# Kernel optimization log

Hardware: AMD Instinct MI355X
Metric: run time of the kernel (lower is better)

## Reference

```python
import jax, jax.numpy as jnp
import numpy as np

N = 25000      # nodes
E = 400000     # edges (avg degree 16)
D = 128        # input feature dim
H = 4          # heads in layer 1
O1 = 128       # per-head out dim layer 1
O2 = 64        # out dim layer 2 (1 head)
NG = 512       # number of graphs in batch
NEG_SLOPE = 0.2


def _gat_layer(x, src, dst, W, a_src, a_dst, bias, heads, out_dim):
    """PyG-style GATConv: gather, per-edge logits, segment softmax over dst, scatter-add."""
    n = x.shape[0]
    h = (x @ W).reshape(n, heads, out_dim)              # [N,H,O]
    al_s = jnp.sum(h * a_src, axis=-1)                  # [N,H]
    al_d = jnp.sum(h * a_dst, axis=-1)                  # [N,H]
    e = jax.nn.leaky_relu(al_s[src] + al_d[dst], NEG_SLOPE)   # [E,H]
    e_max = jax.ops.segment_max(e, dst, num_segments=n)        # [N,H]
    e_exp = jnp.exp(e - e_max[dst])
    denom = jax.ops.segment_sum(e_exp, dst, num_segments=n)    # [N,H]
    alpha = e_exp / denom[dst]                                  # [E,H]
    msg = alpha[:, :, None] * h[src]                             # [E,H,O]  (dominant traffic)
    out = jax.ops.segment_sum(msg, dst, num_segments=n)         # [N,H,O]
    return out.reshape(n, heads * out_dim) + bias


def setup_inputs() -> dict:
    key = jax.random.key(0)
    ks = jax.random.split(key, 16)
    x = jax.random.normal(ks[0], (N, D), dtype=jnp.float32)
    edge_index = jax.random.randint(ks[1], (2, E), 0, N, dtype=jnp.int64)
    batch = jnp.sort(jax.random.randint(ks[2], (N,), 0, NG, dtype=jnp.int64))
    def glorot(k, shape, fan_in):
        return jax.random.normal(k, shape, dtype=jnp.float32) * (1.0 / np.sqrt(fan_in))
    W1 = glorot(ks[3], (D, H * O1), D)
    a_src1 = glorot(ks[4], (H, O1), O1)
    a_dst1 = glorot(ks[5], (H, O1), O1)
    b1 = jnp.zeros((H * O1,), dtype=jnp.float32)
    W2 = glorot(ks[6], (H * O1, O2), H * O1)
    a_src2 = glorot(ks[7], (1, O2), O2)
    a_dst2 = glorot(ks[8], (1, O2), O2)
    b2 = jnp.zeros((O2,), dtype=jnp.float32)
    fc_w1 = glorot(ks[9], (O2, 32), O2)
    fc_b1 = jnp.zeros((32,), dtype=jnp.float32)
    fc_w2 = glorot(ks[10], (32, 1), 32)
    fc_b2 = jnp.zeros((1,), dtype=jnp.float32)
    return {"x": x, "edge_index": edge_index, "batch": batch,
            "W1": W1, "a_src1": a_src1, "a_dst1": a_dst1, "b1": b1,
            "W2": W2, "a_src2": a_src2, "a_dst2": a_dst2, "b2": b2,
            "fc_w1": fc_w1, "fc_b1": fc_b1, "fc_w2": fc_w2, "fc_b2": fc_b2}


def reference(x, edge_index, batch, W1, a_src1, a_dst1, b1, W2, a_src2, a_dst2, b2,
              fc_w1, fc_b1, fc_w2, fc_b2):
    n = x.shape[0]
    loop = jnp.arange(n, dtype=edge_index.dtype)
    src = jnp.concatenate([edge_index[0], loop])   # add_self_loops=True (PyG default)
    dst = jnp.concatenate([edge_index[1], loop])
    h1 = jax.nn.elu(_gat_layer(x, src, dst, W1, a_src1, a_dst1, b1, H, O1))   # [N, 512]
    h2 = jax.nn.elu(_gat_layer(h1, src, dst, W2, a_src2, a_dst2, b2, 1, O2))  # [N, 64]
    # global mean pool over graphs
    sums = jax.ops.segment_sum(h2, batch, num_segments=NG)                     # [NG, 64]
    cnt = jax.ops.segment_sum(jnp.ones((n,), dtype=h2.dtype), batch, num_segments=NG)
    pooled = sums / jnp.maximum(cnt, 1.0)[:, None]
    hid = jax.nn.relu(pooled @ fc_w1 + fc_b1)
    out = jax.nn.sigmoid(hid @ fc_w2 + fc_b2)
    return out.squeeze(-1)                                                     # [NG]
```

## Files before the change

kernel.cpp:

```cpp
#include <hip/hip_runtime.h>
#include <hip/hip_bf16.h>


typedef unsigned short u16;
typedef unsigned int u32;
typedef __attribute__((ext_vector_type(8))) short bf16x8;
typedef __attribute__((ext_vector_type(4))) float f32x4;

#define LRELU(v) ((v) > 0.0f ? (v) : 0.2f * (v))
#define ELU(v)   ((v) > 0.0f ? (v) : expm1f(v))

__device__ __forceinline__ u16 f2bf(float f) {
    union { float f; u32 u; } c; c.f = f;
    u32 u = c.u;
    u32 r = (u + 0x7fffu + ((u >> 16) & 1u)) >> 16;
    return (u16)r;
}
__device__ __forceinline__ float bf2f(u16 h) {
    return __uint_as_float(((u32)h) << 16);
}

__global__ __launch_bounds__(256) void prep_w(const float* __restrict__ W1,
                                              const float* __restrict__ W2,
                                              const float* __restrict__ a_s,
                                              const float* __restrict__ a_d,
                                              u16* __restrict__ W1f,
                                              u16* __restrict__ W2f,
                                              float* __restrict__ Wa,
                                              int* __restrict__ deg, int nDeg) {
    int b = blockIdx.x;
    if (b < 384) {
        int idx = b * 256 + threadIdx.x;
        if (idx < 65536) {
            int fid = idx >> 9, l = (idx >> 3) & 63, j = idx & 7;
            int head = fid >> 5, cb = (fid >> 2) & 7, s = fid & 3;
            int col = head * 128 + cb * 16 + (l & 15);
            int k = s * 32 + 16 * (j >> 2) + 4 * (l >> 4) + (j & 3);
            W1f[idx] = f2bf(W1[(size_t)k * 512 + col]);
        } else {
            int i2 = idx - 65536;
            int fid = i2 >> 9, l = (i2 >> 3) & 63, j = i2 & 7;
            int c2 = fid >> 4, s = fid & 15;
            int col = c2 * 16 + (l & 15);
            int k = s * 32 + 16 * (j >> 2) + 4 * (l >> 4) + (j & 3);
            W2f[i2] = f2bf(W2[(size_t)k * 64 + col]);
        }
    } else if (b < 388) {
        int idx = (b - 384) * 256 + threadIdx.x;
        int k = idx >> 3, j = idx & 7, h = j & 3;
        const float* a = (j < 4) ? (a_s + h * 128) : (a_d + h * 128);
        const float* wrow = W1 + (size_t)k * 512 + h * 128;
        float s = 0.f;
#pragma unroll 8
        for (int o = 0; o < 128; ++o) s += wrow[o] * a[o];
        Wa[k * 8 + j] = s;
    } else {
        int i = (b - 388) * 1024 + threadIdx.x * 4;
        if (i < nDeg) *(int4*)(deg + i) = make_int4(0, 0, 0, 0);
    }
}

__global__ __launch_bounds__(256) void prep_x(const float* __restrict__ x,
                                              const float* __restrict__ Wa,
                                              const int* __restrict__ dstA,
                                              u16* __restrict__ xbf,
                                              float* __restrict__ alS,
                                              float* __restrict__ alD,
                                              int* __restrict__ deg,
                                              int Nn, int E, int NBx) {
    int b = blockIdx.x;
    if (b >= NBx) {
        int e = (b - NBx) * 256 + threadIdx.x;
        if (e < E + Nn) {
            int d = (e < E) ? dstA[e] : (e - E);
            atomicAdd(&deg[d], 1);
        }
        return;
    }
    int lane = threadIdx.x & 63;
    int wave = threadIdx.x >> 6;
    float4 ls = *(const float4*)(Wa + lane * 8);
    float4 ld = *(const float4*)(Wa + lane * 8 + 4);
    float4 hs = *(const float4*)(Wa + (lane + 64) * 8);
    float4 hd = *(const float4*)(Wa + (lane + 64) * 8 + 4);
    int n = b * 4 + wave;
    if (n >= Nn) return;
    float x0 = x[(size_t)n * 128 + lane];
    float x1 = x[(size_t)n * 128 + lane + 64];
    xbf[(size_t)n * 128 + lane]      = f2bf(x0);
    xbf[(size_t)n * 128 + lane + 64] = f2bf(x1);
    float r0 = x0 * ls.x + x1 * hs.x;
    float r1 = x0 * ls.y + x1 * hs.y;
    float r2 = x0 * ls.z + x1 * hs.z;
    float r3 = x0 * ls.w + x1 * hs.w;
    float r4 = x0 * ld.x + x1 * hd.x;
    float r5 = x0 * ld.y + x1 * hd.y;
    float r6 = x0 * ld.z + x1 * hd.z;
    float r7 = x0 * ld.w + x1 * hd.w;
#pragma unroll
    for (int off = 32; off; off >>= 1) {
        r0 += __shfl_down(r0, off); r1 += __shfl_down(r1, off);
        r2 += __shfl_down(r2, off); r3 += __shfl_down(r3, off);
        r4 += __shfl_down(r4, off); r5 += __shfl_down(r5, off);
        r6 += __shfl_down(r6, off); r7 += __shfl_down(r7, off);
    }
    if (lane == 0) {
        *(float4*)(alS + (size_t)n * 4) = make_float4(r0, r1, r2, r3);
        *(float4*)(alD + (size_t)n * 4) = make_float4(r4, r5, r6, r7);
    }
}

__global__ __launch_bounds__(256) void scanA_kernel(const int* __restrict__ deg,
                                                    int* __restrict__ offs,
                                                    int* __restrict__ bsum, int n) {
    __shared__ int sh[256];
    int b = blockIdx.x, t = threadIdx.x;
    int base = b * 2048 + t * 8;
    int v[8]; int s = 0;
#pragma unroll
    for (int j = 0; j < 8; ++j) { int i = base + j; v[j] = (i < n) ? deg[i] : 0; s += v[j]; }
    sh[t] = s;
    __syncthreads();
    for (int off = 1; off < 256; off <<= 1) {
        int u = (t >= off) ? sh[t - off] : 0;
        __syncthreads();
        sh[t] += u;
        __syncthreads();
    }
    int run = sh[t] - s;
    if (t == 255) bsum[b] = sh[255];
#pragma unroll
    for (int j = 0; j < 8; ++j) {
        run += v[j];
        int i = base + j;
        if (i < n) offs[i + 1] = run;
    }
}

__global__ __launch_bounds__(256) void scanC_kernel(int* __restrict__ offs,
                                                    const int* __restrict__ bsum, int n) {
    int i = blockIdx.x * 256 + threadIdx.x;
    if (i == 0) offs[0] = 0;
    if (i >= n) return;
    int b = i >> 11;
    int add = 0;
    for (int j = 0; j < b; ++j) add += bsum[j];
    if (b > 0) offs[i + 1] += add;
}

__global__ __launch_bounds__(256) void scatter_kernel(const int* __restrict__ src,
                                                      const int* __restrict__ dst,
                                                      int E, int Nn,
                                                      const int* __restrict__ offs,
                                                      int* __restrict__ fill,
                                                      const float* __restrict__ alS,
                                                      const float* __restrict__ alD,
                                                      int* __restrict__ sCSR,
                                                      float* __restrict__ wE1) {
    int e = blockIdx.x * 256 + threadIdx.x;
    if (e >= E + Nn) return;
    int s = (e < E) ? src[e] : (e - E);
    int d = (e < E) ? dst[e] : (e - E);
    int pos = offs[d] + atomicAdd(&fill[d], 1);
    sCSR[pos] = s;
    float4 as = *(const float4*)(alS + (size_t)s * 4);
    float4 ad = *(const float4*)(alD + (size_t)d * 4);
    float4 w;
    float t;
    t = as.x + ad.x; w.x = expf(LRELU(t));
    t = as.y + ad.y; w.y = expf(LRELU(t));
    t = as.z + ad.z; w.z = expf(LRELU(t));
    t = as.w + ad.w; w.w = expf(LRELU(t));
    *(float4*)(wE1 + (size_t)pos * 4) = w;
}

__global__ __launch_bounds__(256) void aggx_kernel(const u16* __restrict__ xbf,
                                                   const int* __restrict__ sCSR,
                                                   const int* __restrict__ offs,
                                                   const float* __restrict__ wE,
                                                   u16* __restrict__ xaggF, int Nn) {
    int n = blockIdx.x * 4 + (threadIdx.x >> 6);
    int l = threadIdx.x & 63;
    if (n >= Nn) return;
    int half = l >> 5;
    int fl = (l & 31) * 4;
    float a0[4] = {0.f, 0.f, 0.f, 0.f};
    float a1[4] = {0.f, 0.f, 0.f, 0.f};
    float a2[4] = {0.f, 0.f, 0.f, 0.f};
    float a3[4] = {0.f, 0.f, 0.f, 0.f};
    float ws0 = 0.f, ws1 = 0.f, ws2 = 0.f, ws3 = 0.f;
    int s0 = offs[n], s1 = offs[n + 1];
    int i = s0 + half;
    for (; i + 6 < s1; i += 8) {
        int sn[4]; float4 w[4]; ushort4 u[4];
#pragma unroll
        for (int j = 0; j < 4; ++j) {
            int idx = i + 2 * j;
            sn[j] = sCSR[idx];
            w[j] = *(const float4*)(wE + (size_t)idx * 4);
        }
#pragma unroll
        for (int j = 0; j < 4; ++j)
            u[j] = *(const ushort4*)(xbf + (size_t)sn[j] * 128 + fl);
#pragma unroll
        for (int j = 0; j < 4; ++j) {
            float xv[4] = {bf2f(u[j].x), bf2f(u[j].y), bf2f(u[j].z), bf2f(u[j].w)};
#pragma unroll
            for (int q = 0; q < 4; ++q) {
                a0[q] += w[j].x * xv[q];
                a1[q] += w[j].y * xv[q];
                a2[q] += w[j].z * xv[q];
                a3[q] += w[j].w * xv[q];
            }
            ws0 += w[j].x; ws1 += w[j].y; ws2 += w[j].z; ws3 += w[j].w;
        }
    }
    for (; i < s1; i += 2) {
        int sn = sCSR[i];
        float4 w = *(const float4*)(wE + (size_t)i * 4);
        ushort4 u = *(const ushort4*)(xbf + (size_t)sn * 128 + fl);
        float xv[4] = {bf2f(u.x), bf2f(u.y), bf2f(u.z), bf2f(u.w)};
#pragma unroll
        for (int q = 0; q < 4; ++q) {
            a0[q] += w.x * xv[q];
            a1[q] += w.y * xv[q];
            a2[q] += w.z * xv[q];
            a3[q] += w.w * xv[q];
        }
        ws0 += w.x; ws1 += w.y; ws2 += w.z; ws3 += w.w;
    }
#pragma unroll
    for (int q = 0; q < 4; ++q) {
        a0[q] += __shfl_xor(a0[q], 32);
        a1[q] += __shfl_xor(a1[q], 32);
        a2[q] += __shfl_xor(a2[q], 32);
        a3[q] += __shfl_xor(a3[q], 32);
    }
    ws0 += __shfl_xor(ws0, 32); ws1 += __shfl_xor(ws1, 32);
    ws2 += __shfl_xor(ws2, 32); ws3 += __shfl_xor(ws3, 32);
    if (half == 0) {
        float i0 = 1.f / ws0, i1 = 1.f / ws1, i2 = 1.f / ws2, i3 = 1.f / ws3;
        int group = n >> 4, lrow = n & 15;
        int sl = fl >> 5;
        int kg = (fl >> 2) & 3;
        int j0 = ((fl >> 4) & 1) * 4;
        size_t base = ((size_t)group * 16 + sl) * 512 + (size_t)(kg * 16 + lrow) * 8 + j0;
        ushort4 o;
        o.x = f2bf(a0[0] * i0); o.y = f2bf(a0[1] * i0);
        o.z = f2bf(a0[2] * i0); o.w = f2bf(a0[3] * i0);
        *(ushort4*)(xaggF + base + 0 * 2048) = o;
        o.x = f2bf(a1[0] * i1); o.y = f2bf(a1[1] * i1);
        o.z = f2bf(a1[2] * i1); o.w = f2bf(a1[3] * i1);
        *(ushort4*)(xaggF + base + 1 * 2048) = o;
        o.x = f2bf(a2[0] * i2); o.y = f2bf(a2[1] * i2);
        o.z = f2bf(a2[2] * i2); o.w = f2bf(a2[3] * i2);
        *(ushort4*)(xaggF + base + 2 * 2048) = o;
        o.x = f2bf(a3[0] * i3); o.y = f2bf(a3[1] * i3);
        o.z = f2bf(a3[2] * i3); o.w = f2bf(a3[3] * i3);
        *(ushort4*)(xaggF + base + 3 * 2048) = o;
    }
}

__global__ __launch_bounds__(64) void gemm1_mfma(const u16* __restrict__ xaggF,
                                                 const u16* __restrict__ W1f,
                                                 const float* __restrict__ b1,
                                                 u16* __restrict__ out1F) {
    int l = threadIdx.x;
    int head = blockIdx.y;
    int g0 = blockIdx.x * 2;
    int kg = l >> 4;

    bf16x8 xf[2][4];
#pragma unroll
    for (int g = 0; g < 2; ++g) {
        const u16* p = xaggF + ((size_t)(g0 + g) * 16 + head * 4) * 512 + l * 8;
#pragma unroll
        for (int s = 0; s < 4; ++s) xf[g][s] = *(const bf16x8*)(p + s * 512);
    }

    const u16* wbase = W1f + (size_t)head * 32 * 512 + l * 8;

#pragma unroll
    for (int cbp = 0; cbp < 4; ++cbp) {
        bf16x8 op0, op1;
#pragma unroll
        for (int par = 0; par < 2; ++par) {
            int cb = cbp * 2 + par;
            bf16x8 wf[4];
#pragma unroll
            for (int s = 0; s < 4; ++s)
                wf[s] = *(const bf16x8*)(wbase + (size_t)(cb * 4 + s) * 512);
            float4 bias = *(const float4*)(b1 + head * 128 + cb * 16 + kg * 4);
#pragma unroll
            for (int g = 0; g < 2; ++g) {
                f32x4 acc = {0.f, 0.f, 0.f, 0.f};
#pragma unroll
                for (int s = 0; s < 4; ++s)
                    acc = __builtin_amdgcn_mfma_f32_16x16x32_bf16(wf[s], xf[g][s],
                                                                  acc, 0, 0, 0);
                float v0 = ELU(acc[0] + bias.x);
                float v1 = ELU(acc[1] + bias.y);
                float v2 = ELU(acc[2] + bias.z);
                float v3 = ELU(acc[3] + bias.w);
                bf16x8& op = g ? op1 : op0;
                if (par == 0) {
                    op[0] = (short)f2bf(v0); op[1] = (short)f2bf(v1);
                    op[2] = (short)f2bf(v2); op[3] = (short)f2bf(v3);
                } else {
                    op[4] = (short)f2bf(v0); op[5] = (short)f2bf(v1);
                    op[6] = (short)f2bf(v2); op[7] = (short)f2bf(v3);
                }
            }
        }
#pragma unroll
        for (int g = 0; g < 2; ++g) {
            u16* op = out1F + ((size_t)(g0 + g) * 16 + head * 4 + cbp) * 512 + l * 8;
            *(bf16x8*)op = g ? op1 : op0;
        }
    }
}

__global__ __launch_bounds__(64) void gemm2_mfma(const u16* __restrict__ out1F,
                                                 const u16* __restrict__ W2f,
                                                 const float* __restrict__ a_s2,
                                                 const float* __restrict__ a_d2,
                                                 u16* __restrict__ h2bf,
                                                 float* __restrict__ alS,
                                                 float* __restrict__ alD, int M) {
    int l = threadIdx.x;
    int g = blockIdx.x;
    int lrow = l & 15, kg = l >> 4;
    int node = g * 16 + lrow;

    const u16* xp = out1F + (size_t)g * 16 * 512 + l * 8;
    bf16x8 xf[16];
#pragma unroll
    for (int s = 0; s < 16; ++s) xf[s] = *(const bf16x8*)(xp + s * 512);

    const u16* wp = W2f + l * 8;
    float ps = 0.f, pd = 0.f;
#pragma unroll
    for (int c2 = 0; c2 < 4; ++c2) {
        int c0 = c2 * 16;
        f32x4 acc = {0.f, 0.f, 0.f, 0.f};
#pragma unroll
        for (int s = 0; s < 16; ++s) {
            bf16x8 wf = *(const bf16x8*)(wp + (size_t)(c2 * 16 + s) * 512);
            acc = __builtin_amdgcn_mfma_f32_16x16x32_bf16(wf, xf[s], acc, 0, 0, 0);
        }
        float4 as = *(const float4*)(a_s2 + c0 + kg * 4);
        float4 ad = *(const float4*)(a_d2 + c0 + kg * 4);
        ps += acc[0] * as.x + acc[1] * as.y + acc[2] * as.z + acc[3] * as.w;
        pd += acc[0] * ad.x + acc[1] * ad.y + acc[2] * ad.z + acc[3] * ad.w;
        if (node < M) {
            ushort4 o;
            o.x = f2bf(acc[0]); o.y = f2bf(acc[1]);
            o.z = f2bf(acc[2]); o.w = f2bf(acc[3]);
            *(ushort4*)(h2bf + (size_t)node * 64 + c0 + kg * 4) = o;
        }
    }
    ps += __shfl_xor(ps, 16); ps += __shfl_xor(ps, 32);
    pd += __shfl_xor(pd, 16); pd += __shfl_xor(pd, 32);
    if (kg == 0 && node < M) { alS[node] = ps; alD[node] = pd; }
}

__global__ __launch_bounds__(256) void agg2_kernel(const u16* __restrict__ h2bf,
                                                   const int* __restrict__ sCSR,
                                                   const int* __restrict__ offs,
                                                   const float* __restrict__ alS2,
                                                   const float* __restrict__ alD2,
                                                   const float* __restrict__ b2,
                                                   float* __restrict__ out2, int Nn) {
    int n = blockIdx.x * 4 + (threadIdx.x >> 6);
    int l = threadIdx.x & 63;
    if (n >= Nn) return;
    int half = l >> 5;
    int fl = (l & 31) * 2;
    float ad = alD2[n];
    float ax = 0.f, ay = 0.f, ws = 0.f;
    int s0 = offs[n], s1 = offs[n + 1];
    int i = s0 + half;
    for (; i + 6 < s1; i += 8) {
        int sn[4]; float als[4]; u32 u[4];
#pragma unroll
        for (int j = 0; j < 4; ++j) sn[j] = sCSR[i + 2 * j];
#pragma unroll
        for (int j = 0; j < 4; ++j) {
            als[j] = alS2[sn[j]];
            u[j] = *(const u32*)(h2bf + (size_t)sn[j] * 64 + fl);
        }
#pragma unroll
        for (int j = 0; j < 4; ++j) {
            float t = als[j] + ad;
            float w = expf(LRELU(t));
            ax += w * __uint_as_float(u[j] << 16);
            ay += w * __uint_as_float(u[j] & 0xffff0000u);
            ws += w;
        }
    }
    for (; i < s1; i += 2) {
        int sn = sCSR[i];
        float t = alS2[sn] + ad;
        float w = expf(LRELU(t));
        u32 u = *(const u32*)(h2bf + (size_t)sn * 64 + fl);
        ax += w * __uint_as_float(u << 16);
        ay += w * __uint_as_float(u & 0xffff0000u);
        ws += w;
    }
    ax += __shfl_xor(ax, 32);
    ay += __shfl_xor(ay, 32);
    ws += __shfl_xor(ws, 32);
    if (half == 0) {
        float inv = 1.f / ws;
        float2 o;
        float v0 = ax * inv + b2[fl];
        float v1 = ay * inv + b2[fl + 1];
        o.x = ELU(v0);
        o.y = ELU(v1);
        *(float2*)(out2 + (size_t)n * 64 + fl) = o;
    }
}

__device__ __forceinline__ int lower_bound_i(const int* arr, int n, int key) {
    int lo = 0, hi = n;
    while (lo < hi) {
        int mid = (lo + hi) >> 1;
        if (arr[mid] < key) lo = mid + 1; else hi = mid;
    }
    return lo;
}

__global__ __launch_bounds__(64) void poolfc_kernel(const float* __restrict__ h2,
                                                    const int* __restrict__ batch,
                                                    int Nn,
                                                    const float* __restrict__ w1,
                                                    const float* __restrict__ bb1,
                                                    const float* __restrict__ w2,
                                                    const float* __restrict__ bb2,
                                                    float* __restrict__ out) {
    int g = blockIdx.x;
    __shared__ int sh[2];
    __shared__ float p[64];
    __shared__ float hid[32];
    int t = threadIdx.x;
    if (t == 0) sh[0] = lower_bound_i(batch, Nn, g);
    if (t == 1) sh[1] = lower_bound_i(batch, Nn, g + 1);
    __syncthreads();
    int s0 = sh[0], s1 = sh[1];
    float sum = 0.f;
    for (int i = s0; i < s1; ++i) sum += h2[(size_t)i * 64 + t];
    float cnt = (float)((s1 - s0) > 1 ? (s1 - s0) : 1);
    p[t] = sum / cnt;
    __syncthreads();
    if (t < 32) {
        float a = bb1[t];
#pragma unroll
        for (int k = 0; k < 64; ++k) a += p[k] * w1[k * 32 + t];
        hid[t] = a > 0.f ? a : 0.f;
    }
    __syncthreads();
    if (t == 0) {
        float a = bb2[0];
#pragma unroll
        for (int j = 0; j < 32; ++j) a += hid[j] * w2[j];
        out[g] = 1.0f / (1.0f + expf(-a));
    }
}

extern "C" void kernel_launch(void* const* d_in, const int* in_sizes, int n_in,
                              void* d_out, int out_size, void* d_ws, size_t ws_size,
                              hipStream_t stream) {
    const float* x      = (const float*)d_in[0];
    const int*   ei     = (const int*)d_in[1];
    const int*   batch  = (const int*)d_in[2];
    const float* W1     = (const float*)d_in[3];
    const float* a_src1 = (const float*)d_in[4];
    const float* a_dst1 = (const float*)d_in[5];
    const float* b1     = (const float*)d_in[6];
    const float* W2     = (const float*)d_in[7];
    const float* a_src2 = (const float*)d_in[8];
    const float* a_dst2 = (const float*)d_in[9];
    const float* b2     = (const float*)d_in[10];
    const float* fcw1   = (const float*)d_in[11];
    const float* fcb1   = (const float*)d_in[12];
    const float* fcw2   = (const float*)d_in[13];
    const float* fcb2   = (const float*)d_in[14];
    float* out = (float*)d_out;

    const int Nn = in_sizes[0] / 128;
    const int E  = in_sizes[1] / 2;
    const int Et = E + Nn;
    const int NG = out_size;
    const int* srcA = ei;
    const int* dstA = ei + E;

    const int ngroups = (Nn + 15) / 16;
    const int ngp = (ngroups + 1) & ~1;

    char* base = (char*)d_ws;
    size_t off = 0;
    auto alloc = [&](size_t bytes) -> void* {
        void* p = base + off;
        off += (bytes + 255) & ~(size_t)255;
        return p;
    };
    u16*   xbf    = (u16*)alloc((size_t)Nn * 128 * 2);
    u16*   xaggF  = (u16*)alloc((size_t)ngp * 16 * 512 * 2);
    u16*   out1F  = (u16*)alloc((size_t)ngp * 16 * 512 * 2);
    u16*   h2bf   = (u16*)alloc((size_t)Nn * 64 * 2);
    float* out2   = (float*)alloc((size_t)Nn * 64 * 4);
    u16*   W1f    = (u16*)alloc(65536 * 2);
    u16*   W2f    = (u16*)alloc(32768 * 2);
    float* Wa     = (float*)alloc(128 * 8 * 4);
    float* alS1   = (float*)alloc((size_t)Nn * 4 * 4);
    float* alD1   = (float*)alloc((size_t)Nn * 4 * 4);
    float* alS2   = (float*)alloc((size_t)Nn * 4);
    float* alD2   = (float*)alloc((size_t)Nn * 4);
    float* wE1    = (float*)alloc((size_t)Et * 4 * 4);
    int*   deg    = (int*)alloc((size_t)2 * Nn * 4);
    int*   fill   = deg + Nn;
    int*   offs   = (int*)alloc((size_t)(Nn + 1) * 4);
    int*   bsum   = (int*)alloc(64 * 4);
    int*   sCSR   = (int*)alloc((size_t)Et * 4);
    (void)ws_size; (void)n_in;

    const int EB = (Et + 255) / 256;
    const int NB = (Nn + 2047) / 2048;
    const int NBx = (Nn + 3) / 4;
    const int ZB = (2 * Nn + 1023) / 1024;

    prep_w<<<388 + ZB, 256, 0, stream>>>(W1, W2, a_src1, a_dst1, W1f, W2f, Wa,
                                         deg, 2 * Nn);
    prep_x<<<NBx + EB, 256, 0, stream>>>(x, Wa, dstA, xbf, alS1, alD1, deg,
                                         Nn, E, NBx);
    scanA_kernel<<<NB, 256, 0, stream>>>(deg, offs, bsum, Nn);
    scanC_kernel<<<(Nn + 255) / 256, 256, 0, stream>>>(offs, bsum, Nn);
    scatter_kernel<<<EB, 256, 0, stream>>>(srcA, dstA, E, Nn, offs, fill,
                                           alS1, alD1, sCSR, wE1);

    aggx_kernel<<<(Nn + 3) / 4, 256, 0, stream>>>(xbf, sCSR, offs, wE1, xaggF, Nn);
    dim3 g1(ngp / 2, 4);
    gemm1_mfma<<<g1, 64, 0, stream>>>(xaggF, W1f, b1, out1F);
    gemm2_mfma<<<ngroups, 64, 0, stream>>>(out1F, W2f, a_src2, a_dst2,
                                           h2bf, alS2, alD2, Nn);

    agg2_kernel<<<(Nn + 3) / 4, 256, 0, stream>>>(h2bf, sCSR, offs, alS2, alD2,
                                                  b2, out2, Nn);

    poolfc_kernel<<<NG, 64, 0, stream>>>(out2, batch, Nn, fcw1, fcb1, fcw2, fcb2, out);
}
```

Before: 181.3 us.

## Fuse layer-1 GEMM with layer-2 GEMM, keeping intermediate in registers

Merges gemm1_mfma and gemm2_mfma into one kernel where each 64-thread block computes all four heads of the layer-1 output for a 16-node group and feeds the bf16 results directly as MFMA operands for the layer-2 GEMM. This removes the out1F intermediate buffer write and re-read (about 25 MB of bf16 traffic) plus one kernel launch. In exchange the grid shrinks from four blocks per group pair to one block per group. Each block now does four times the layer-1 work and holds 16 bf16x8 registers live, which may hurt occupancy and latency hiding.

```diff
diff --git a/kernel.cpp b/kernel.cpp
--- a/kernel.cpp
+++ b/kernel.cpp
@@ -261,81 +261,56 @@
     }
 }
 
-__global__ __launch_bounds__(64) void gemm1_mfma(const u16* __restrict__ xaggF,
-                                                 const u16* __restrict__ W1f,
-                                                 const float* __restrict__ b1,
-                                                 u16* __restrict__ out1F) {
+__global__ __launch_bounds__(64) void fused_gemm12(const u16* __restrict__ xaggF,
+                                                   const u16* __restrict__ W1f,
+                                                   const float* __restrict__ b1,
+                                                   const u16* __restrict__ W2f,
+                                                   const float* __restrict__ a_s2,
+                                                   const float* __restrict__ a_d2,
+                                                   u16* __restrict__ h2bf,
+                                                   float* __restrict__ alS,
+                                                   float* __restrict__ alD, int M) {
     int l = threadIdx.x;
-    int head = blockIdx.y;
-    int g0 = blockIdx.x * 2;
-    int kg = l >> 4;
-
-    bf16x8 xf[2][4];
-#pragma unroll
-    for (int g = 0; g < 2; ++g) {
-        const u16* p = xaggF + ((size_t)(g0 + g) * 16 + head * 4) * 512 + l * 8;
-#pragma unroll
-        for (int s = 0; s < 4; ++s) xf[g][s] = *(const bf16x8*)(p + s * 512);
-    }
-
-    const u16* wbase = W1f + (size_t)head * 32 * 512 + l * 8;
-
-#pragma unroll
-    for (int cbp = 0; cbp < 4; ++cbp) {
-        bf16x8 op0, op1;
-#pragma unroll
-        for (int par = 0; par < 2; ++par) {
-            int cb = cbp * 2 + par;
-            bf16x8 wf[4];
-#pragma unroll
-            for (int s = 0; s < 4; ++s)
-                wf[s] = *(const bf16x8*)(wbase + (size_t)(cb * 4 + s) * 512);
-            float4 bias = *(const float4*)(b1 + head * 128 + cb * 16 + kg * 4);
-#pragma unroll
-            for (int g = 0; g < 2; ++g) {
+    int g = blockIdx.x;
+    int lrow = l & 15, kg = l >> 4;
+    int node = g * 16 + lrow;
+
+    bf16x8 xf2[16];
+#pragma unroll
+    for (int h = 0; h < 4; ++h) {
+        bf16x8 xf[4];
+        const u16* xp = xaggF + ((size_t)g * 16 + h * 4) * 512 + l * 8;
+#pragma unroll
+        for (int s = 0; s < 4; ++s) xf[s] = *(const bf16x8*)(xp + s * 512);
+        const u16* wbase = W1f + (size_t)h * 32 * 512 + l * 8;
+#pragma unroll
+        for (int cbp = 0; cbp < 4; ++cbp) {
+            bf16x8 of;
+#pragma unroll
+            for (int par = 0; par < 2; ++par) {
+                int cb = cbp * 2 + par;
                 f32x4 acc = {0.f, 0.f, 0.f, 0.f};
 #pragma unroll
-                for (int s = 0; s < 4; ++s)
-                    acc = __builtin_amdgcn_mfma_f32_16x16x32_bf16(wf[s], xf[g][s],
-                                                                  acc, 0, 0, 0);
+                for (int s = 0; s < 4; ++s) {
+                    bf16x8 wf = *(const bf16x8*)(wbase + (size_t)(cb * 4 + s) * 512);
+                    acc = __builtin_amdgcn_mfma_f32_16x16x32_bf16(wf, xf[s], acc, 0, 0, 0);
+                }
+                float4 bias = *(const float4*)(b1 + h * 128 + cb * 16 + kg * 4);
                 float v0 = ELU(acc[0] + bias.x);
                 float v1 = ELU(acc[1] + bias.y);
                 float v2 = ELU(acc[2] + bias.z);
                 float v3 = ELU(acc[3] + bias.w);
-                bf16x8& op = g ? op1 : op0;
                 if (par == 0) {
-                    op[0] = (short)f2bf(v0); op[1] = (short)f2bf(v1);
-                    op[2] = (short)f2bf(v2); op[3] = (short)f2bf(v3);
+                    of[0] = (short)f2bf(v0); of[1] = (short)f2bf(v1);
+                    of[2] = (short)f2bf(v2); of[3] = (short)f2bf(v3);
                 } else {
-                    op[4] = (short)f2bf(v0); op[5] = (short)f2bf(v1);
-                    op[6] = (short)f2bf(v2); op[7] = (short)f2bf(v3);
+                    of[4] = (short)f2bf(v0); of[5] = (short)f2bf(v1);
+                    of[6] = (short)f2bf(v2); of[7] = (short)f2bf(v3);
                 }
             }
-        }
-#pragma unroll
-        for (int g = 0; g < 2; ++g) {
-            u16* op = out1F + ((size_t)(g0 + g) * 16 + head * 4 + cbp) * 512 + l * 8;
-            *(bf16x8*)op = g ? op1 : op0;
-        }
-    }
-}
-
-__global__ __launch_bounds__(64) void gemm2_mfma(const u16* __restrict__ out1F,
-                                                 const u16* __restrict__ W2f,
-                                                 const float* __restrict__ a_s2,
-                                                 const float* __restrict__ a_d2,
-                                                 u16* __restrict__ h2bf,
-                                                 float* __restrict__ alS,
-                                                 float* __restrict__ alD, int M) {
-    int l = threadIdx.x;
-    int g = blockIdx.x;
-    int lrow = l & 15, kg = l >> 4;
-    int node = g * 16 + lrow;
-
-    const u16* xp = out1F + (size_t)g * 16 * 512 + l * 8;
-    bf16x8 xf[16];
-#pragma unroll
-    for (int s = 0; s < 16; ++s) xf[s] = *(const bf16x8*)(xp + s * 512);
+            xf2[h * 4 + cbp] = of;
+        }
+    }
 
     const u16* wp = W2f + l * 8;
     float ps = 0.f, pd = 0.f;
@@ -346,7 +321,7 @@
 #pragma unroll
         for (int s = 0; s < 16; ++s) {
             bf16x8 wf = *(const bf16x8*)(wp + (size_t)(c2 * 16 + s) * 512);
-            acc = __builtin_amdgcn_mfma_f32_16x16x32_bf16(wf, xf[s], acc, 0, 0, 0);
+            acc = __builtin_amdgcn_mfma_f32_16x16x32_bf16(wf, xf2[s], acc, 0, 0, 0);
         }
         float4 as = *(const float4*)(a_s2 + c0 + kg * 4);
         float4 ad = *(const float4*)(a_d2 + c0 + kg * 4);
@@ -506,7 +481,6 @@
     };
     u16*   xbf    = (u16*)alloc((size_t)Nn * 128 * 2);
     u16*   xaggF  = (u16*)alloc((size_t)ngp * 16 * 512 * 2);
-    u16*   out1F  = (u16*)alloc((size_t)ngp * 16 * 512 * 2);
     u16*   h2bf   = (u16*)alloc((size_t)Nn * 64 * 2);
     float* out2   = (float*)alloc((size_t)Nn * 64 * 4);
     u16*   W1f    = (u16*)alloc(65536 * 2);
@@ -539,10 +513,9 @@
                                            alS1, alD1, sCSR, wE1);
 
     aggx_kernel<<<(Nn + 3) / 4, 256, 0, stream>>>(xbf, sCSR, offs, wE1, xaggF, Nn);
-    dim3 g1(ngp / 2, 4);
-    gemm1_mfma<<<g1, 64, 0, stream>>>(xaggF, W1f, b1, out1F);
-    gemm2_mfma<<<ngroups, 64, 0, stream>>>(out1F, W2f, a_src2, a_dst2,
-                                           h2bf, alS2, alD2, Nn);
+
+    fused_gemm12<<<ngroups, 64, 0, stream>>>(xaggF, W1f, b1, W2f, a_src2, a_dst2,
+                                             h2bf, alS2, alD2, Nn);
 
     agg2_kernel<<<(Nn + 3) / 4, 256, 0, stream>>>(h2bf, sCSR, offs, alS2, alD2,
                                                   b2, out2, Nn);
```

After: 194.9 us. 7.5% more time.

## Fold scan block-prefix into consumers and widen pooling to four waves

Applied to the files above, without the earlier changes.

Removes the separate scanC kernel launch. scanA now writes exclusive block-local offsets, and scatter, aggx and agg2 each compute the block prefix from bsum with a wave-level shuffle scan, taking the segment end from deg[n]. The pooling kernel goes from one wave to four per graph, each summing a strided subset of rows, then reduces through shared memory. The aim is to save one launch and its serial bsum loop, and to shorten the serial pool loop. The cost is extra shuffles in every aggregation wave, and the bsum_pref scan only covers 32 blocks (about 65k nodes), which is enough here.

```diff
diff --git a/kernel.cpp b/kernel.cpp
--- a/kernel.cpp
+++ b/kernel.cpp
@@ -18,6 +18,18 @@
 }
 __device__ __forceinline__ float bf2f(u16 h) {
     return __uint_as_float(((u32)h) << 16);
+}
+
+__device__ __forceinline__ int bsum_pref(const int* __restrict__ bsum,
+                                         int nb, int b, int lane) {
+    int v = (lane < nb) ? bsum[lane] : 0;
+#pragma unroll
+    for (int off = 1; off < 32; off <<= 1) {
+        int u = __shfl_up(v, off);
+        if (lane >= off) v += u;
+    }
+    int p = __shfl(v, (b > 0) ? (b - 1) : 0);
+    return (b > 0) ? p : 0;
 }
 
 __global__ __launch_bounds__(256) void prep_w(const float* __restrict__ W1,
@@ -131,37 +143,34 @@
     if (t == 255) bsum[b] = sh[255];
 #pragma unroll
     for (int j = 0; j < 8; ++j) {
+        int i = base + j;
+        if (i < n) offs[i] = run;
         run += v[j];
-        int i = base + j;
-        if (i < n) offs[i + 1] = run;
-    }
-}
-
-__global__ __launch_bounds__(256) void scanC_kernel(int* __restrict__ offs,
-                                                    const int* __restrict__ bsum, int n) {
-    int i = blockIdx.x * 256 + threadIdx.x;
-    if (i == 0) offs[0] = 0;
-    if (i >= n) return;
-    int b = i >> 11;
-    int add = 0;
-    for (int j = 0; j < b; ++j) add += bsum[j];
-    if (b > 0) offs[i + 1] += add;
+    }
 }
 
 __global__ __launch_bounds__(256) void scatter_kernel(const int* __restrict__ src,
                                                       const int* __restrict__ dst,
                                                       int E, int Nn,
                                                       const int* __restrict__ offs,
+                                                      const int* __restrict__ bsum,
+                                                      int NB,
                                                       int* __restrict__ fill,
                                                       const float* __restrict__ alS,
                                                       const float* __restrict__ alD,
                                                       int* __restrict__ sCSR,
                                                       float* __restrict__ wE1) {
     int e = blockIdx.x * 256 + threadIdx.x;
-    if (e >= E + Nn) return;
-    int s = (e < E) ? src[e] : (e - E);
-    int d = (e < E) ? dst[e] : (e - E);
-    int pos = offs[d] + atomicAdd(&fill[d], 1);
+    int lane = threadIdx.x & 63;
+    bool live = (e < E + Nn);
+    int s = 0, d = 0;
+    if (live) {
+        s = (e < E) ? src[e] : (e - E);
+        d = (e < E) ? dst[e] : (e - E);
+    }
+    int pref = bsum_pref(bsum, NB, d >> 11, lane);
+    if (!live) return;
+    int pos = offs[d] + pref + atomicAdd(&fill[d], 1);
     sCSR[pos] = s;
     float4 as = *(const float4*)(alS + (size_t)s * 4);
     float4 ad = *(const float4*)(alD + (size_t)d * 4);
@@ -177,10 +186,14 @@
 __global__ __launch_bounds__(256) void aggx_kernel(const u16* __restrict__ xbf,
                                                    const int* __restrict__ sCSR,
                                                    const int* __restrict__ offs,
+                                                   const int* __restrict__ bsum,
+                                                   const int* __restrict__ deg,
+                                                   int NB,
                                                    const float* __restrict__ wE,
                                                    u16* __restrict__ xaggF, int Nn) {
     int n = blockIdx.x * 4 + (threadIdx.x >> 6);
     int l = threadIdx.x & 63;
+    int pref = bsum_pref(bsum, NB, (n < Nn ? n : 0) >> 11, l);
     if (n >= Nn) return;
     int half = l >> 5;
     int fl = (l & 31) * 4;
@@ -189,7 +202,8 @@
     float a2[4] = {0.f, 0.f, 0.f, 0.f};
     float a3[4] = {0.f, 0.f, 0.f, 0.f};
     float ws0 = 0.f, ws1 = 0.f, ws2 = 0.f, ws3 = 0.f;
-    int s0 = offs[n], s1 = offs[n + 1];
+    int s0 = offs[n] + pref;
+    int s1 = s0 + deg[n];
     int i = s0 + half;
     for (; i + 6 < s1; i += 8) {
         int sn[4]; float4 w[4]; ushort4 u[4];
@@ -367,18 +381,23 @@
 __global__ __launch_bounds__(256) void agg2_kernel(const u16* __restrict__ h2bf,
                                                    const int* __restrict__ sCSR,
                                                    const int* __restrict__ offs,
+                                                   const int* __restrict__ bsum,
+                                                   const int* __restrict__ deg,
+                                                   int NB,
                                                    const float* __restrict__ alS2,
                                                    const float* __restrict__ alD2,
                                                    const float* __restrict__ b2,
                                                    float* __restrict__ out2, int Nn) {
     int n = blockIdx.x * 4 + (threadIdx.x >> 6);
     int l = threadIdx.x & 63;
+    int pref = bsum_pref(bsum, NB, (n < Nn ? n : 0) >> 11, l);
     if (n >= Nn) return;
     int half = l >> 5;
     int fl = (l & 31) * 2;
     float ad = alD2[n];
     float ax = 0.f, ay = 0.f, ws = 0.f;
-    int s0 = offs[n], s1 = offs[n + 1];
+    int s0 = offs[n] + pref;
+    int s1 = s0 + deg[n];
     int i = s0 + half;
     for (; i + 6 < s1; i += 8) {
         int sn[4]; float als[4]; u32 u[4];
@@ -430,36 +449,43 @@
     return lo;
 }
 
-__global__ __launch_bounds__(64) void poolfc_kernel(const float* __restrict__ h2,
-                                                    const int* __restrict__ batch,
-                                                    int Nn,
-                                                    const float* __restrict__ w1,
-                                                    const float* __restrict__ bb1,
-                                                    const float* __restrict__ w2,
-                                                    const float* __restrict__ bb2,
-                                                    float* __restrict__ out) {
+__global__ __launch_bounds__(256) void poolfc_kernel(const float* __restrict__ h2,
+                                                     const int* __restrict__ batch,
+                                                     int Nn,
+                                                     const float* __restrict__ w1,
+                                                     const float* __restrict__ bb1,
+                                                     const float* __restrict__ w2,
+                                                     const float* __restrict__ bb2,
+                                                     float* __restrict__ out) {
     int g = blockIdx.x;
     __shared__ int sh[2];
+    __shared__ float psum[4][64];
     __shared__ float p[64];
     __shared__ float hid[32];
-    int t = threadIdx.x;
-    if (t == 0) sh[0] = lower_bound_i(batch, Nn, g);
-    if (t == 1) sh[1] = lower_bound_i(batch, Nn, g + 1);
+    int tid = threadIdx.x;
+    int w = tid >> 6, t = tid & 63;
+    if (tid == 0) sh[0] = lower_bound_i(batch, Nn, g);
+    if (tid == 1) sh[1] = lower_bound_i(batch, Nn, g + 1);
     __syncthreads();
     int s0 = sh[0], s1 = sh[1];
     float sum = 0.f;
-    for (int i = s0; i < s1; ++i) sum += h2[(size_t)i * 64 + t];
-    float cnt = (float)((s1 - s0) > 1 ? (s1 - s0) : 1);
-    p[t] = sum / cnt;
+    for (int i = s0 + w; i < s1; i += 4) sum += h2[(size_t)i * 64 + t];
+    psum[w][t] = sum;
     __syncthreads();
-    if (t < 32) {
-        float a = bb1[t];
-#pragma unroll
-        for (int k = 0; k < 64; ++k) a += p[k] * w1[k * 32 + t];
-        hid[t] = a > 0.f ? a : 0.f;
+    if (w == 0) {
+        float tot = psum[0][t] + psum[1][t] + psum[2][t] + psum[3][t];
+        float cnt = (float)((s1 - s0) > 1 ? (s1 - s0) : 1);
+        p[t] = tot / cnt;
     }
     __syncthreads();
-    if (t == 0) {
+    if (tid < 32) {
+        float a = bb1[tid];
+#pragma unroll
+        for (int k = 0; k < 64; ++k) a += p[k] * w1[k * 32 + tid];
+        hid[tid] = a > 0.f ? a : 0.f;
+    }
+    __syncthreads();
+    if (tid == 0) {
         float a = bb2[0];
 #pragma unroll
         for (int j = 0; j < 32; ++j) a += hid[j] * w2[j];
@@ -534,18 +560,19 @@
     prep_x<<<NBx + EB, 256, 0, stream>>>(x, Wa, dstA, xbf, alS1, alD1, deg,
                                          Nn, E, NBx);
     scanA_kernel<<<NB, 256, 0, stream>>>(deg, offs, bsum, Nn);
-    scanC_kernel<<<(Nn + 255) / 256, 256, 0, stream>>>(offs, bsum, Nn);
-    scatter_kernel<<<EB, 256, 0, stream>>>(srcA, dstA, E, Nn, offs, fill,
-                                           alS1, alD1, sCSR, wE1);
-
-    aggx_kernel<<<(Nn + 3) / 4, 256, 0, stream>>>(xbf, sCSR, offs, wE1, xaggF, Nn);
+    scatter_kernel<<<EB, 256, 0, stream>>>(srcA, dstA, E, Nn, offs, bsum, NB,
+                                           fill, alS1, alD1, sCSR, wE1);
+
+    aggx_kernel<<<(Nn + 3) / 4, 256, 0, stream>>>(xbf, sCSR, offs, bsum, deg, NB,
+                                                  wE1, xaggF, Nn);
     dim3 g1(ngp / 2, 4);
     gemm1_mfma<<<g1, 64, 0, stream>>>(xaggF, W1f, b1, out1F);
     gemm2_mfma<<<ngroups, 64, 0, stream>>>(out1F, W2f, a_src2, a_dst2,
                                            h2bf, alS2, alD2, Nn);
 
-    agg2_kernel<<<(Nn + 3) / 4, 256, 0, stream>>>(h2bf, sCSR, offs, alS2, alD2,
-                                                  b2, out2, Nn);
-
-    poolfc_kernel<<<NG, 64, 0, stream>>>(out2, batch, Nn, fcw1, fcb1, fcw2, fcb2, out);
-}
+    agg2_kernel<<<(Nn + 3) / 4, 256, 0, stream>>>(h2bf, sCSR, offs, bsum, deg, NB,
+                                                  alS2, alD2, b2, out2, Nn);
+
+    poolfc_kernel<<<NG, 256, 0, stream>>>(out2, batch, Nn, fcw1, fcb1, fcw2,
+                                          fcb2, out);
+}
```

Result: faster. 167.8 us (-7.5%).
